# Kernel optimization log

Measured on AMD Instinct MI355X. Metric: run time of the kernel, lower is better.

## Reference

```python
import jax, jax.numpy as jnp
import numpy as np

DIM, HEADS, DIM_HEAD = 1024, 16, 64
INNER = HEADS * DIM_HEAD
B, N = 2, 2048


def setup_inputs() -> dict:
    key = jax.random.key(0)
    ks = jax.random.split(key, 9)
    w = lambda k, shape: (jax.random.normal(k, shape, dtype=jnp.float32) * 0.02)
    return {
        "x": jax.random.normal(ks[0], (B, N, DIM), dtype=jnp.float32),
        "y": jax.random.normal(ks[1], (B, N, DIM), dtype=jnp.float32),
        "z": jax.random.normal(ks[2], (B, N, DIM), dtype=jnp.float32),
        "w_sa1": w(ks[3], (DIM, INNER)),
        "w_sa2": w(ks[4], (DIM, INNER)),
        "w_se1": w(ks[5], (DIM, INNER)),
        "w_se2": w(ks[6], (DIM, INNER)),
        "w_out": w(ks[7], (INNER, DIM)),
        "b_out": jnp.zeros((DIM,), dtype=jnp.float32),
    }


def reference(x, y, z, w_sa1, w_sa2, w_se1, w_se2, w_out, b_out):
    b, n, _ = x.shape
    h, d = HEADS, DIM_HEAD
    scale = d ** -0.5

    def split_heads(t):  # [b,n,h*d] -> [b,h,n,d]
        return t.reshape(b, n, h, d).transpose(0, 2, 1, 3)

    z1 = split_heads(z @ w_sa1)
    yh = split_heads(y @ w_sa2)
    xh = split_heads(x @ w_se1)
    z2 = split_heads(z @ w_se2)

    # spatial attention: [b,h,n,n], softmax over keys (last dim)
    sacm = jax.nn.softmax(jnp.einsum('bhid,bhjd->bhij', z1, yh) * scale, axis=-1)
    # channel attention: [b,h,d,d], extra 1/(n/d) scaling, softmax over last dim
    secm = jax.nn.softmax(
        jnp.einsum('bhni,bhnj->bhij', xh, z2) * scale / (n / d), axis=-1)

    out1 = jnp.einsum('bhij,bhjd->bhid', sacm, xh)  # [b,h,n,d]
    out2 = jnp.einsum('bhni,bhij->bhnj', yh, secm)  # [b,h,n,d]

    out = (out1 + out2).transpose(0, 2, 1, 3).reshape(b, n, h * d)
    return out @ w_out + b_out  # dropout=0.0 -> identity
```

## Files before the change

kernel.cpp:

```cpp
#include <hip/hip_runtime.h>


typedef unsigned short u16;
typedef unsigned int u32;
typedef __attribute__((ext_vector_type(8))) short bf16x8;
typedef __attribute__((ext_vector_type(4))) float f32x4;

#define DEV __device__ __forceinline__

DEV u16 f2bf(float f) {
  unsigned u = __builtin_bit_cast(unsigned, f);
  u += 0x7FFFu + ((u >> 16) & 1u);
  return (u16)(u >> 16);
}
DEV float bf2f(u16 h) {
  unsigned u = ((unsigned)h) << 16;
  return __builtin_bit_cast(float, u);
}

DEV void gld16(const void* g, void* l) {
  __builtin_amdgcn_global_load_lds(
      (const __attribute__((address_space(1))) unsigned int*)g,
      (__attribute__((address_space(3))) unsigned int*)l, 16, 0, 0);
}

union B8 {
  u32 w[4];
  bf16x8 v;
};

__global__ __launch_bounds__(256) void cvt_kernel(const float* __restrict__ in,
                                                  u16* __restrict__ out) {
  const int i = blockIdx.x * 256 + threadIdx.x;
  float4 v = ((const float4*)in)[i];
  u16 o[4] = {f2bf(v.x), f2bf(v.y), f2bf(v.z), f2bf(v.w)};
  ((ushort4*)out)[i] = *(const ushort4*)o;
}

__global__ __launch_bounds__(256) void wtT_kernel(const float* __restrict__ W,
                                                  u16* __restrict__ Wt) {
  __shared__ float tile[32][33];
  const int k0 = blockIdx.x * 32, c0 = blockIdx.y * 32;
  const int tx = threadIdx.x & 31, ty = threadIdx.x >> 5;
#pragma unroll
  for (int i = 0; i < 32; i += 8)
    tile[ty + i][tx] = W[(size_t)(k0 + ty + i) * 1024 + c0 + tx];
  __syncthreads();
#pragma unroll
  for (int i = 0; i < 32; i += 8)
    Wt[(size_t)(c0 + ty + i) * 1024 + k0 + tx] = f2bf(tile[tx][ty + i]);
}

template <int EPI>
__global__ __launch_bounds__(256, 2) void gemm128(const u16* __restrict__ A,
                                                  const u16* __restrict__ Bt,
                                                  void* __restrict__ Cout,
                                                  const float* __restrict__ bias,
                                                  int M, int K, float oscale) {
  __shared__ __align__(16) u16 Ab[128 * 32];
  __shared__ __align__(16) u16 Bb[128 * 32];
  const int tid = threadIdx.x;
  const int lane = tid & 63, wv = tid >> 6;
  const int g = lane >> 4, c = lane & 15;
  const int m0 = blockIdx.x * 128, n0 = blockIdx.y * 128;
  const int wr = (wv >> 1) * 64, wc = (wv & 1) * 64;
  const int srow = lane >> 2, scol = (lane & 3) * 8;

  f32x4 acc[4][4];
#pragma unroll
  for (int i = 0; i < 4; i++)
#pragma unroll
    for (int j = 0; j < 4; j++) acc[i][j] = f32x4{0.f, 0.f, 0.f, 0.f};

  for (int k0 = 0; k0 < K; k0 += 32) {
    __syncthreads();
#pragma unroll
    for (int i = 0; i < 2; i++) {
      const int ch = wv + i * 4;
      gld16(&A[(size_t)(m0 + ch * 16 + srow) * K + k0 + scol], &Ab[ch * 512]);
      gld16(&Bt[(size_t)(n0 + ch * 16 + srow) * K + k0 + scol], &Bb[ch * 512]);
    }
    __syncthreads();
    bf16x8 af[4], bf[4];
#pragma unroll
    for (int mi = 0; mi < 4; mi++)
      af[mi] = *(const bf16x8*)&Ab[(wr + mi * 16 + c) * 32 + g * 8];
#pragma unroll
    for (int ni = 0; ni < 4; ni++)
      bf[ni] = *(const bf16x8*)&Bb[(wc + ni * 16 + c) * 32 + g * 8];
#pragma unroll
    for (int mi = 0; mi < 4; mi++)
#pragma unroll
      for (int ni = 0; ni < 4; ni++)
        acc[mi][ni] = __builtin_amdgcn_mfma_f32_16x16x32_bf16(af[mi], bf[ni],
                                                              acc[mi][ni], 0, 0, 0);
  }

#pragma unroll
  for (int mi = 0; mi < 4; mi++)
#pragma unroll
    for (int ni = 0; ni < 4; ni++)
#pragma unroll
      for (int r = 0; r < 4; r++) {
        const int m = m0 + wr + mi * 16 + g * 4 + r;
        const int n = n0 + wc + ni * 16 + c;
        if constexpr (EPI == 0) {
          const int b = m >> 11, nn = m & 2047, h = n >> 6, d = n & 63;
          ((u16*)Cout)[((((size_t)(b * 16 + h)) * 2048 + nn) << 6) + d] =
              f2bf(acc[mi][ni][r] * oscale);
        } else {
          ((float*)Cout)[(size_t)m * 1024 + n] = acc[mi][ni][r] + bias[n];
        }
      }
}

__global__ __launch_bounds__(256, 2) void attn_sp(const u16* __restrict__ Q,
                                                  const u16* __restrict__ K,
                                                  const u16* __restrict__ V,
                                                  u16* __restrict__ comb) {
  __shared__ __align__(16) u16 Kld[2][4096];
  __shared__ __align__(16) u16 Vld[2][4096];
  const int tid = threadIdx.x, lane = tid & 63, wv = tid >> 6;
  const int g = lane >> 4, c = lane & 15;
  const int bh = blockIdx.x & 31, qt = blockIdx.x >> 5;
  const size_t base = (size_t)bh * (2048 * 64);
  const int q0 = qt * 128 + wv * 32;
  const u16* Qp = Q + base;
  const u16* Kp = K + base;
  const u16* Vp = V + base;

  bf16x8 qf[2][2];
#pragma unroll
  for (int qb = 0; qb < 2; qb++)
#pragma unroll
    for (int kf = 0; kf < 2; kf++)
      qf[qb][kf] =
          *(const bf16x8*)&Qp[(size_t)(q0 + qb * 16 + c) * 64 + kf * 32 + g * 8];

  int ksrc[2], kbas[2];
#pragma unroll
  for (int t2 = 0; t2 < 2; t2++) {
    const int r = wv * 16 + t2 * 8 + (lane >> 3);
    const int ul = (lane & 7) ^ (lane >> 3) ^ ((wv * 2 + t2) & 7);
    ksrc[t2] = r * 64 + ul * 8;
    kbas[t2] = wv * 1024 + t2 * 512;
  }
  const int vd0 = (lane & 7) * 8;
  const int vkey0 = wv * 8 + (lane >> 3), vkey1 = 32 + vkey0;
  const int vx = lane & 7;

  f32x4 acc[2][4];
  float mrow[2] = {-3e38f, -3e38f}, lrow[2] = {0.f, 0.f};
#pragma unroll
  for (int qb = 0; qb < 2; qb++)
#pragma unroll
    for (int df = 0; df < 4; df++) acc[qb][df] = f32x4{0.f, 0.f, 0.f, 0.f};

  gld16(Kp + ksrc[0], &Kld[0][kbas[0]]);
  gld16(Kp + ksrc[1], &Kld[0][kbas[1]]);
  int4 vv0 = *(const int4*)&Vp[(size_t)vkey0 * 64 + vd0];
  int4 vv1 = *(const int4*)&Vp[(size_t)vkey1 * 64 + vd0];

  for (int t = 0; t < 32; ++t) {
    const int p = t & 1;
    u16* Kb = Kld[p];
    u16* Vb = Vld[p];
    __syncthreads();

    {
      const u16* vs = (const u16*)&vv0;
      const int ui = wv, si = vkey0 & 7;
#pragma unroll
      for (int j = 0; j < 8; j++)
        Vb[(vd0 + j) * 64 + (((ui ^ j ^ vx) & 7) << 3) + si] = vs[j];
    }
    {
      const u16* vs = (const u16*)&vv1;
      const int ui = 4 + wv, si = vkey1 & 7;
#pragma unroll
      for (int j = 0; j < 8; j++)
        Vb[(vd0 + j) * 64 + (((ui ^ j ^ vx) & 7) << 3) + si] = vs[j];
    }
    if (t < 31) {
      const u16* Kn = Kp + (t + 1) * 4096;
      gld16(Kn + ksrc[0], &Kld[p ^ 1][kbas[0]]);
      gld16(Kn + ksrc[1], &Kld[p ^ 1][kbas[1]]);
      const u16* Vn = Vp + (t + 1) * 4096;
      vv0 = *(const int4*)&Vn[vkey0 * 64 + vd0];
      vv1 = *(const int4*)&Vn[vkey1 * 64 + vd0];
    }

    f32x4 st[2][4];
#pragma unroll
    for (int qb = 0; qb < 2; qb++)
#pragma unroll
      for (int nf = 0; nf < 4; nf++) st[qb][nf] = f32x4{0.f, 0.f, 0.f, 0.f};
#pragma unroll
    for (int nf = 0; nf < 4; nf++)
#pragma unroll
      for (int kf = 0; kf < 2; kf++) {
        const int phys = (kf * 4 + g) ^ (c & 7) ^ ((nf * 2 + (c >> 3)) & 7);
        bf16x8 af =
            *(const bf16x8*)((const char*)Kb + ((nf * 16 + c) << 7) + (phys << 4));
        st[0][nf] = __builtin_amdgcn_mfma_f32_16x16x32_bf16(af, qf[0][kf],
                                                            st[0][nf], 0, 0, 0);
        st[1][nf] = __builtin_amdgcn_mfma_f32_16x16x32_bf16(af, qf[1][kf],
                                                            st[1][nf], 0, 0, 0);
      }

    u32 pk[2][4][2];
#pragma unroll
    for (int qb = 0; qb < 2; qb++) {
      float mt = -3e38f;
#pragma unroll
      for (int nf = 0; nf < 4; nf++)
#pragma unroll
        for (int r = 0; r < 4; r++) mt = fmaxf(mt, st[qb][nf][r]);
      mt = fmaxf(mt, __shfl_xor(mt, 16));
      mt = fmaxf(mt, __shfl_xor(mt, 32));
      const float mnew = fmaxf(mrow[qb], mt);
      const float fsc = __expf(mrow[qb] - mnew);
      mrow[qb] = mnew;
      float p_[4][4];
      float ps = 0.f;
#pragma unroll
      for (int nf = 0; nf < 4; nf++)
#pragma unroll
        for (int r = 0; r < 4; r++) {
          p_[nf][r] = __expf(st[qb][nf][r] - mnew);
          ps += p_[nf][r];
        }
      ps += __shfl_xor(ps, 16);
      ps += __shfl_xor(ps, 32);
      lrow[qb] = lrow[qb] * fsc + ps;
      float fo[4];
#pragma unroll
      for (int r = 0; r < 4; r++) fo[r] = __shfl(fsc, 4 * g + r);
#pragma unroll
      for (int df = 0; df < 4; df++)
#pragma unroll
        for (int r = 0; r < 4; r++) acc[qb][df][r] *= fo[r];
#pragma unroll
      for (int nf = 0; nf < 4; nf++) {
        pk[qb][nf][0] = (u32)f2bf(p_[nf][0]) | ((u32)f2bf(p_[nf][1]) << 16);
        pk[qb][nf][1] = (u32)f2bf(p_[nf][2]) | ((u32)f2bf(p_[nf][3]) << 16);
      }
    }
    __syncthreads();

#pragma unroll
    for (int kk = 0; kk < 2; kk++) {
      const int srcA = c + ((g & 1) << 5);
      const int srcB = srcA + 16;
      const bool hi = g >= 2;
      bf16x8 pf[2];
#pragma unroll
      for (int qb = 0; qb < 2; qb++) {
        B8 u;
        u32 a0 = (u32)__shfl((int)pk[qb][2 * kk + 0][0], srcA);
        u32 a1 = (u32)__shfl((int)pk[qb][2 * kk + 1][0], srcA);
        u.w[0] = hi ? a1 : a0;
        a0 = (u32)__shfl((int)pk[qb][2 * kk + 0][1], srcA);
        a1 = (u32)__shfl((int)pk[qb][2 * kk + 1][1], srcA);
        u.w[1] = hi ? a1 : a0;
        a0 = (u32)__shfl((int)pk[qb][2 * kk + 0][0], srcB);
        a1 = (u32)__shfl((int)pk[qb][2 * kk + 1][0], srcB);
        u.w[2] = hi ? a1 : a0;
        a0 = (u32)__shfl((int)pk[qb][2 * kk + 0][1], srcB);
        a1 = (u32)__shfl((int)pk[qb][2 * kk + 1][1], srcB);
        u.w[3] = hi ? a1 : a0;
        pf[qb] = u.v;
      }
#pragma unroll
      for (int df = 0; df < 4; df++) {
        const int phys = (kk * 4 + g) ^ (c & 7) ^ ((df * 2 + (c >> 3)) & 7);
        bf16x8 vf =
            *(const bf16x8*)((const char*)Vb + ((df * 16 + c) << 7) + (phys << 4));
        acc[0][df] = __builtin_amdgcn_mfma_f32_16x16x32_bf16(pf[0], vf,
                                                             acc[0][df], 0, 0, 0);
        acc[1][df] = __builtin_amdgcn_mfma_f32_16x16x32_bf16(pf[1], vf,
                                                             acc[1][df], 0, 0, 0);
      }
    }
  }

  const int b = bh >> 4, h = bh & 15;
#pragma unroll
  for (int qb = 0; qb < 2; qb++)
#pragma unroll
    for (int r = 0; r < 4; r++) {
      const float lr = __shfl(lrow[qb], 4 * g + r);
      const float inv = 1.f / lr;
      const int n = q0 + qb * 16 + g * 4 + r;
      const size_t off = ((size_t)(b * 2048 + n)) * 1024 + h * 64;
#pragma unroll
      for (int df = 0; df < 4; df++)
        comb[off + df * 16 + c] = f2bf(acc[qb][df][r] * inv);
    }
}

__global__ __launch_bounds__(256) void chan_part(const u16* __restrict__ Xh,
                                                 const u16* __restrict__ Z2,
                                                 float* __restrict__ part) {
  const int bh = blockIdx.y, sl = blockIdx.x;
  const size_t base = (size_t)bh * (2048 * 64);
  const int ti = threadIdx.x >> 4, tj = threadIdx.x & 15;
  float a[4][4];
#pragma unroll
  for (int u = 0; u < 4; u++)
#pragma unroll
    for (int v = 0; v < 4; v++) a[u][v] = 0.f;
  const int n0 = sl * 256;
  for (int n = 0; n < 256; n++) {
    ushort4 xv = *(const ushort4*)&Xh[base + (size_t)(n0 + n) * 64 + ti * 4];
    ushort4 zv = *(const ushort4*)&Z2[base + (size_t)(n0 + n) * 64 + tj * 4];
    float xf[4] = {bf2f(xv.x), bf2f(xv.y), bf2f(xv.z), bf2f(xv.w)};
    float zf[4] = {bf2f(zv.x), bf2f(zv.y), bf2f(zv.z), bf2f(zv.w)};
#pragma unroll
    for (int u = 0; u < 4; u++)
#pragma unroll
      for (int v = 0; v < 4; v++) a[u][v] += xf[u] * zf[v];
  }
  float* dst = part + ((size_t)bh * 8 + sl) * 4096;
#pragma unroll
  for (int u = 0; u < 4; u++)
#pragma unroll
    for (int v = 0; v < 4; v++) dst[(ti * 4 + u) * 64 + tj * 4 + v] = a[u][v];
}

__global__ __launch_bounds__(64) void chan_sm(const float* __restrict__ part,
                                              float* __restrict__ secm) {
  const int bh = blockIdx.x, r = threadIdx.x;
  float v[64];
#pragma unroll
  for (int j = 0; j < 64; j++) v[j] = 0.f;
  for (int sl = 0; sl < 8; sl++) {
    const float* p = part + ((size_t)bh * 8 + sl) * 4096 + r * 64;
#pragma unroll
    for (int j = 0; j < 64; j++) v[j] += p[j];
  }
  float mx = -1e30f;
#pragma unroll
  for (int j = 0; j < 64; j++) {
    v[j] *= (1.f / 256.f);
    mx = fmaxf(mx, v[j]);
  }
  float sum = 0.f;
#pragma unroll
  for (int j = 0; j < 64; j++) {
    v[j] = __expf(v[j] - mx);
    sum += v[j];
  }
  const float inv = 1.f / sum;
  float* o = secm + (size_t)bh * 4096 + r * 64;
#pragma unroll
  for (int j = 0; j < 64; j++) o[j] = v[j] * inv;
}

__global__ __launch_bounds__(256) void combine_k(const u16* __restrict__ Yh,
                                                 const float* __restrict__ secm,
                                                 u16* __restrict__ comb) {
  const int tid = threadIdx.x, lane = tid & 63, wv = tid >> 6;
  const size_t row = (size_t)blockIdx.x * 4 + wv;
  const int bh = (int)(row >> 11), n = (int)(row & 2047);
  const int b = bh >> 4, h = bh & 15;
  const float yv = bf2f(Yh[row * 64 + lane]);
  const float* S = secm + (size_t)bh * 4096;
  float acc2 = 0.f;
#pragma unroll 8
  for (int i = 0; i < 64; i++) acc2 += __shfl(yv, i) * S[i * 64 + lane];
  const size_t off = ((size_t)(b * 2048 + n)) * 1024 + (size_t)h * 64 + lane;
  comb[off] = f2bf(bf2f(comb[off]) + acc2);
}

extern "C" void kernel_launch(void* const* d_in, const int* in_sizes, int n_in,
                              void* d_out, int out_size, void* d_ws, size_t ws_size,
                              hipStream_t stream) {
  (void)in_sizes; (void)n_in; (void)out_size; (void)ws_size;
  const float* x = (const float*)d_in[0];
  const float* y = (const float*)d_in[1];
  const float* z = (const float*)d_in[2];
  const float* w_sa1 = (const float*)d_in[3];
  const float* w_sa2 = (const float*)d_in[4];
  const float* w_se1 = (const float*)d_in[5];
  const float* w_se2 = (const float*)d_in[6];
  const float* w_out = (const float*)d_in[7];
  const float* b_out = (const float*)d_in[8];

  char* w = (char*)d_ws;
  const size_t MB = (size_t)1 << 20;
  u16* xb = (u16*)(w + 0);
  u16* comb = xb;
  u16* yb = (u16*)(w + 8 * MB);
  float* scpart = (float*)(w + 8 * MB);
  u16* zb = (u16*)(w + 16 * MB);
  float* secm = (float*)(w + 16 * MB);
  u16* Wt1 = (u16*)(w + 24 * MB);
  u16* Wt2 = (u16*)(w + 26 * MB);
  u16* Wt3 = (u16*)(w + 28 * MB);
  u16* Wt4 = (u16*)(w + 30 * MB);
  u16* Wto = (u16*)(w + 32 * MB);
  u16* z1 = (u16*)(w + 34 * MB);
  u16* yh = (u16*)(w + 42 * MB);
  u16* xh = (u16*)(w + 50 * MB);
  u16* z2 = (u16*)(w + 58 * MB);

  cvt_kernel<<<4096, 256, 0, stream>>>(x, xb);
  cvt_kernel<<<4096, 256, 0, stream>>>(y, yb);
  cvt_kernel<<<4096, 256, 0, stream>>>(z, zb);
  dim3 tg(32, 32);
  wtT_kernel<<<tg, 256, 0, stream>>>(w_sa1, Wt1);
  wtT_kernel<<<tg, 256, 0, stream>>>(w_sa2, Wt2);
  wtT_kernel<<<tg, 256, 0, stream>>>(w_se1, Wt3);
  wtT_kernel<<<tg, 256, 0, stream>>>(w_se2, Wt4);
  wtT_kernel<<<tg, 256, 0, stream>>>(w_out, Wto);
  dim3 gg(32, 8);
  gemm128<0><<<gg, 256, 0, stream>>>(zb, Wt1, z1, nullptr, 4096, 1024, 0.125f);
  gemm128<0><<<gg, 256, 0, stream>>>(yb, Wt2, yh, nullptr, 4096, 1024, 1.0f);
  gemm128<0><<<gg, 256, 0, stream>>>(xb, Wt3, xh, nullptr, 4096, 1024, 1.0f);
  gemm128<0><<<gg, 256, 0, stream>>>(zb, Wt4, z2, nullptr, 4096, 1024, 1.0f);
  attn_sp<<<512, 256, 0, stream>>>(z1, yh, xh, comb);
  chan_part<<<dim3(8, 32), 256, 0, stream>>>(xh, z2, scpart);
  chan_sm<<<32, 64, 0, stream>>>(scpart, secm);
  combine_k<<<16384, 256, 0, stream>>>(yh, secm, comb);
  gemm128<1><<<gg, 256, 0, stream>>>(comb, Wto, d_out, b_out, 4096, 1024, 1.0f);
}
```

Measured before the change: 432.6 us.

## Batch four projection GEMMs into one launch and add lazy softmax rescaling

The four separate Q/K/V/Z projection GEMM launches become one 32x32-grid kernel. It picks the activation matrix and scale per projection from blockIdx.y and relies on the transposed weights and head-split outputs sitting contiguously in the workspace. This should fill the GPU better than four 256-block launches and removes launch gaps. The attention softmax also skips the running-max update and accumulator rescale whenever the new tile max stays within 8 of the old max, which trades some exp range headroom for fewer shuffles and multiplies.

```diff
diff --git a/kernel.cpp b/kernel.cpp
--- a/kernel.cpp
+++ b/kernel.cpp
@@ -51,12 +51,73 @@
     Wt[(size_t)(c0 + ty + i) * 1024 + k0 + tx] = f2bf(tile[tx][ty + i]);
 }
 
-template <int EPI>
-__global__ __launch_bounds__(256, 2) void gemm128(const u16* __restrict__ A,
-                                                  const u16* __restrict__ Bt,
-                                                  void* __restrict__ Cout,
-                                                  const float* __restrict__ bias,
-                                                  int M, int K, float oscale) {
+__global__ __launch_bounds__(256, 2) void gemm_proj(const u16* __restrict__ Az,
+                                                    const u16* __restrict__ Ay,
+                                                    const u16* __restrict__ Ax,
+                                                    const u16* __restrict__ Bt,
+                                                    u16* __restrict__ out) {
+  __shared__ __align__(16) u16 Ab[128 * 32];
+  __shared__ __align__(16) u16 Bb[128 * 32];
+  const int tid = threadIdx.x;
+  const int lane = tid & 63, wv = tid >> 6;
+  const int g = lane >> 4, c = lane & 15;
+  const int m0 = blockIdx.x * 128, n0 = blockIdx.y * 128;
+  const int proj = blockIdx.y >> 3;
+  const u16* A = (proj == 1) ? Ay : (proj == 2) ? Ax : Az;
+  const float oscale = (proj == 0) ? 0.125f : 1.0f;
+  const int wr = (wv >> 1) * 64, wc = (wv & 1) * 64;
+  const int srow = lane >> 2, scol = (lane & 3) * 8;
+
+  f32x4 acc[4][4];
+#pragma unroll
+  for (int i = 0; i < 4; i++)
+#pragma unroll
+    for (int j = 0; j < 4; j++) acc[i][j] = f32x4{0.f, 0.f, 0.f, 0.f};
+
+  for (int k0 = 0; k0 < 1024; k0 += 32) {
+    __syncthreads();
+#pragma unroll
+    for (int i = 0; i < 2; i++) {
+      const int ch = wv + i * 4;
+      gld16(&A[(size_t)(m0 + ch * 16 + srow) * 1024 + k0 + scol], &Ab[ch * 512]);
+      gld16(&Bt[(size_t)(n0 + ch * 16 + srow) * 1024 + k0 + scol], &Bb[ch * 512]);
+    }
+    __syncthreads();
+    bf16x8 af[4], bf[4];
+#pragma unroll
+    for (int mi = 0; mi < 4; mi++)
+      af[mi] = *(const bf16x8*)&Ab[(wr + mi * 16 + c) * 32 + g * 8];
+#pragma unroll
+    for (int ni = 0; ni < 4; ni++)
+      bf[ni] = *(const bf16x8*)&Bb[(wc + ni * 16 + c) * 32 + g * 8];
+#pragma unroll
+    for (int mi = 0; mi < 4; mi++)
+#pragma unroll
+      for (int ni = 0; ni < 4; ni++)
+        acc[mi][ni] = __builtin_amdgcn_mfma_f32_16x16x32_bf16(af[mi], bf[ni],
+                                                              acc[mi][ni], 0, 0, 0);
+  }
+
+#pragma unroll
+  for (int mi = 0; mi < 4; mi++)
+#pragma unroll
+    for (int ni = 0; ni < 4; ni++)
+#pragma unroll
+      for (int r = 0; r < 4; r++) {
+        const int m = m0 + wr + mi * 16 + g * 4 + r;
+        const int ng = n0 + wc + ni * 16 + c;
+        const int nl = ng & 1023;
+        const int b = m >> 11, nn = m & 2047, h = nl >> 6, d = nl & 63;
+        out[(size_t)proj * 4194304 +
+            ((((size_t)(b * 16 + h)) * 2048 + nn) << 6) + d] =
+            f2bf(acc[mi][ni][r] * oscale);
+      }
+}
+
+__global__ __launch_bounds__(256, 2) void gemm_out(const u16* __restrict__ A,
+                                                   const u16* __restrict__ Bt,
+                                                   float* __restrict__ Cout,
+                                                   const float* __restrict__ bias) {
   __shared__ __align__(16) u16 Ab[128 * 32];
   __shared__ __align__(16) u16 Bb[128 * 32];
   const int tid = threadIdx.x;
@@ -72,13 +133,13 @@
 #pragma unroll
     for (int j = 0; j < 4; j++) acc[i][j] = f32x4{0.f, 0.f, 0.f, 0.f};
 
-  for (int k0 = 0; k0 < K; k0 += 32) {
+  for (int k0 = 0; k0 < 1024; k0 += 32) {
     __syncthreads();
 #pragma unroll
     for (int i = 0; i < 2; i++) {
       const int ch = wv + i * 4;
-      gld16(&A[(size_t)(m0 + ch * 16 + srow) * K + k0 + scol], &Ab[ch * 512]);
-      gld16(&Bt[(size_t)(n0 + ch * 16 + srow) * K + k0 + scol], &Bb[ch * 512]);
+      gld16(&A[(size_t)(m0 + ch * 16 + srow) * 1024 + k0 + scol], &Ab[ch * 512]);
+      gld16(&Bt[(size_t)(n0 + ch * 16 + srow) * 1024 + k0 + scol], &Bb[ch * 512]);
     }
     __syncthreads();
     bf16x8 af[4], bf[4];
@@ -104,13 +165,7 @@
       for (int r = 0; r < 4; r++) {
         const int m = m0 + wr + mi * 16 + g * 4 + r;
         const int n = n0 + wc + ni * 16 + c;
-        if constexpr (EPI == 0) {
-          const int b = m >> 11, nn = m & 2047, h = n >> 6, d = n & 63;
-          ((u16*)Cout)[((((size_t)(b * 16 + h)) * 2048 + nn) << 6) + d] =
-              f2bf(acc[mi][ni][r] * oscale);
-        } else {
-          ((float*)Cout)[(size_t)m * 1024 + n] = acc[mi][ni][r] + bias[n];
-        }
+        Cout[(size_t)m * 1024 + n] = acc[mi][ni][r] + bias[n];
       }
 }
 
@@ -218,28 +273,41 @@
         for (int r = 0; r < 4; r++) mt = fmaxf(mt, st[qb][nf][r]);
       mt = fmaxf(mt, __shfl_xor(mt, 16));
       mt = fmaxf(mt, __shfl_xor(mt, 32));
-      const float mnew = fmaxf(mrow[qb], mt);
-      const float fsc = __expf(mrow[qb] - mnew);
-      mrow[qb] = mnew;
       float p_[4][4];
       float ps = 0.f;
-#pragma unroll
-      for (int nf = 0; nf < 4; nf++)
-#pragma unroll
-        for (int r = 0; r < 4; r++) {
-          p_[nf][r] = __expf(st[qb][nf][r] - mnew);
-          ps += p_[nf][r];
-        }
-      ps += __shfl_xor(ps, 16);
-      ps += __shfl_xor(ps, 32);
-      lrow[qb] = lrow[qb] * fsc + ps;
-      float fo[4];
-#pragma unroll
-      for (int r = 0; r < 4; r++) fo[r] = __shfl(fsc, 4 * g + r);
-#pragma unroll
-      for (int df = 0; df < 4; df++)
-#pragma unroll
-        for (int r = 0; r < 4; r++) acc[qb][df][r] *= fo[r];
+      if (__all(mt <= mrow[qb] + 8.0f)) {
+#pragma unroll
+        for (int nf = 0; nf < 4; nf++)
+#pragma unroll
+          for (int r = 0; r < 4; r++) {
+            p_[nf][r] = __expf(st[qb][nf][r] - mrow[qb]);
+            ps += p_[nf][r];
+          }
+        ps += __shfl_xor(ps, 16);
+        ps += __shfl_xor(ps, 32);
+        lrow[qb] += ps;
+      } else {
+        const float mnew = fmaxf(mrow[qb], mt);
+        const float fsc = __expf(mrow[qb] - mnew);
+        mrow[qb] = mnew;
+#pragma unroll
+        for (int nf = 0; nf < 4; nf++)
+#pragma unroll
+          for (int r = 0; r < 4; r++) {
+            p_[nf][r] = __expf(st[qb][nf][r] - mnew);
+            ps += p_[nf][r];
+          }
+        ps += __shfl_xor(ps, 16);
+        ps += __shfl_xor(ps, 32);
+        lrow[qb] = lrow[qb] * fsc + ps;
+        float fo[4];
+#pragma unroll
+        for (int r = 0; r < 4; r++) fo[r] = __shfl(fsc, 4 * g + r);
+#pragma unroll
+        for (int df = 0; df < 4; df++)
+#pragma unroll
+          for (int r = 0; r < 4; r++) acc[qb][df][r] *= fo[r];
+      }
 #pragma unroll
       for (int nf = 0; nf < 4; nf++) {
         pk[qb][nf][0] = (u32)f2bf(p_[nf][0]) | ((u32)f2bf(p_[nf][1]) << 16);
@@ -414,14 +482,12 @@
   wtT_kernel<<<tg, 256, 0, stream>>>(w_se1, Wt3);
   wtT_kernel<<<tg, 256, 0, stream>>>(w_se2, Wt4);
   wtT_kernel<<<tg, 256, 0, stream>>>(w_out, Wto);
-  dim3 gg(32, 8);
-  gemm128<0><<<gg, 256, 0, stream>>>(zb, Wt1, z1, nullptr, 4096, 1024, 0.125f);
-  gemm128<0><<<gg, 256, 0, stream>>>(yb, Wt2, yh, nullptr, 4096, 1024, 1.0f);
-  gemm128<0><<<gg, 256, 0, stream>>>(xb, Wt3, xh, nullptr, 4096, 1024, 1.0f);
-  gemm128<0><<<gg, 256, 0, stream>>>(zb, Wt4, z2, nullptr, 4096, 1024, 1.0f);
+  dim3 gp(32, 32);
+  gemm_proj<<<gp, 256, 0, stream>>>(zb, yb, xb, Wt1, z1);
   attn_sp<<<512, 256, 0, stream>>>(z1, yh, xh, comb);
   chan_part<<<dim3(8, 32), 256, 0, stream>>>(xh, z2, scpart);
   chan_sm<<<32, 64, 0, stream>>>(scpart, secm);
   combine_k<<<16384, 256, 0, stream>>>(yh, secm, comb);
-  gemm128<1><<<gg, 256, 0, stream>>>(comb, Wto, d_out, b_out, 4096, 1024, 1.0f);
-}
+  dim3 gg(32, 8);
+  gemm_out<<<gg, 256, 0, stream>>>(comb, Wto, (float*)d_out, b_out);
+}
```

Result: faster. 367.1 us (-15.2%).
